# Kernel tuning notes

Measured on AMD Instinct MI355X. Metric: run time of the kernel, lower is better.

The kernel has to match this reference:

```python
import jax, jax.numpy as jnp
import numpy as np

D_MODEL = 1024
N_HEADS = 16
D_K = D_MODEL // N_HEADS
THETA = 10000.0
MAX_SEQ_LEN = 2048


def _rope_tables(seq_len):
    pos = jnp.arange(seq_len, dtype=jnp.float32)
    inv_freq = 1.0 / (THETA ** (jnp.arange(0, D_K, 2, dtype=jnp.float32) / D_K))
    ang = pos[:, None] * inv_freq[None, :]  # [T, D_K/2]
    return jnp.cos(ang), jnp.sin(ang)


def _apply_rope(x, cos, sin):
    # x: [..., T, D_K]; cos/sin: [T, D_K/2]
    x_even = x[..., ::2]
    x_odd = x[..., 1::2]
    r_even = x_even * cos - x_odd * sin
    r_odd = x_even * sin + x_odd * cos
    out = jnp.stack([r_even, r_odd], axis=-1)  # [..., T, D_K/2, 2]
    return out.reshape(x.shape)


def setup_inputs() -> dict:
    key = jax.random.key(0)
    ks = jax.random.split(key, 5)
    std = np.sqrt(2.0 / (D_MODEL + D_MODEL))
    x = jax.random.normal(ks[0], (2, 2048, D_MODEL), dtype=jnp.float32)
    w_q = jax.random.normal(ks[1], (D_MODEL, D_MODEL), dtype=jnp.float32) * std
    w_k = jax.random.normal(ks[2], (D_MODEL, D_MODEL), dtype=jnp.float32) * std
    w_v = jax.random.normal(ks[3], (D_MODEL, D_MODEL), dtype=jnp.float32) * std
    w_o = jax.random.normal(ks[4], (D_MODEL, D_MODEL), dtype=jnp.float32) * std
    return {"x": x, "w_q": w_q, "w_k": w_k, "w_v": w_v, "w_o": w_o}


def reference(x, w_q, w_k, w_v, w_o):
    B, T, _ = x.shape
    # projections: weight stored as [d_out, d_in], y = x @ W^T
    q = jnp.einsum('btd,od->bto', x, w_q)
    k = jnp.einsum('btd,od->bto', x, w_k)
    v = jnp.einsum('btd,od->bto', x, w_v)
    # split heads: [B, T, H*Dk] -> [B, H, T, Dk]
    q = q.reshape(B, T, N_HEADS, D_K).transpose(0, 2, 1, 3)
    k = k.reshape(B, T, N_HEADS, D_K).transpose(0, 2, 1, 3)
    v = v.reshape(B, T, N_HEADS, D_K).transpose(0, 2, 1, 3)
    cos, sin = _rope_tables(T)
    q = _apply_rope(q, cos, sin)
    k = _apply_rope(k, cos, sin)
    scores = jnp.einsum('bhqd,bhkd->bhqk', q, k) / np.sqrt(D_K).astype(np.float32)
    causal = jnp.tril(jnp.ones((T, T), dtype=bool))
    scores = jnp.where(causal, scores, -jnp.inf)
    attn = jax.nn.softmax(scores, axis=-1)
    out = jnp.einsum('bhqk,bhkd->bhqd', attn, v)
    out = out.transpose(0, 2, 1, 3).reshape(B, T, D_MODEL)
    return jnp.einsum('btd,od->bto', out, w_o)
```

## Files before the change

### kernel.cpp

```cpp
#include <hip/hip_runtime.h>
#include <hip/hip_bf16.h>

typedef __bf16 bf16_t;
typedef __bf16 bf16x8 __attribute__((ext_vector_type(8)));
typedef float f32x4 __attribute__((ext_vector_type(4)));
typedef short short4v __attribute__((ext_vector_type(4)));
typedef unsigned int uint2v __attribute__((ext_vector_type(2)));

#define D_MODEL 1024
#define T_SEQ 2048
#define NH 16
#define DKD 64
#define X_ELEMS (4194304u)
#define W_ELEMS (1048576u)
#define Q_SCALE 0.18033688011112042f

__device__ __forceinline__ void async16(const bf16_t* g, bf16_t* l) {
    __builtin_amdgcn_global_load_lds((const __attribute__((address_space(1))) void*)g,
                                     (__attribute__((address_space(3))) void*)l, 16, 0, 0);
}

__device__ __forceinline__ unsigned ldsa(const bf16_t* p) {
    return (unsigned)(size_t)(const __attribute__((address_space(3))) bf16_t*)p;
}

__global__ __launch_bounds__(256) void convert_kernel(
    const float* __restrict__ x, const float* __restrict__ wq,
    const float* __restrict__ wk, const float* __restrict__ wv,
    const float* __restrict__ wo,
    bf16_t* __restrict__ xb, bf16_t* __restrict__ wqb, bf16_t* __restrict__ wkb,
    bf16_t* __restrict__ wvb, bf16_t* __restrict__ wob,
    float* __restrict__ cost, float* __restrict__ sint)
{
    const unsigned bid = blockIdx.x;
    if (bid < 8192) {
        size_t idx = ((size_t)bid * 256 + threadIdx.x) * 4;
        const float* src; bf16_t* dst; size_t off;
        if (idx < X_ELEMS) { src = x; dst = xb; off = idx; }
        else {
            size_t r = idx - X_ELEMS;
            unsigned w = (unsigned)(r >> 20);
            off = r & (W_ELEMS - 1);
            src = (w == 0) ? wq : (w == 1) ? wk : (w == 2) ? wv : wo;
            dst = (w == 0) ? wqb : (w == 1) ? wkb : (w == 2) ? wvb : wob;
        }
        float4 v = *(const float4*)(src + off);
        union { bf16_t b[4]; short4v s; } u;
        u.b[0] = (bf16_t)v.x; u.b[1] = (bf16_t)v.y;
        u.b[2] = (bf16_t)v.z; u.b[3] = (bf16_t)v.w;
        *(short4v*)(dst + off) = u.s;
    } else {
        int idx = (int)(bid - 8192) * 256 + threadIdx.x;
        int t = idx >> 5, i = idx & 31;
        float inv = expf(-0.28782313662425572f * (float)i);
        float ang = (float)t * inv;
        float s, c;
        sincosf(ang, &s, &c);
        cost[idx] = c; sint[idx] = s;
    }
}

__global__ __launch_bounds__(256) void gemm_fused(
    const bf16_t* __restrict__ A,
    const bf16_t* __restrict__ W0, const bf16_t* __restrict__ W1, const bf16_t* __restrict__ W2,
    bf16_t* __restrict__ qout, bf16_t* __restrict__ kout, bf16_t* __restrict__ vout,
    const float* __restrict__ cost, const float* __restrict__ sint,
    float* __restrict__ fout, int modeBase)
{
    const int K = 1024;
    __shared__ bf16_t As[128 * 32];
    __shared__ bf16_t Bs[128 * 32];
    const int tid = threadIdx.x;
    const int wave = tid >> 6, lane = tid & 63;
    const int quad = lane >> 4, l16 = lane & 15;
    const int m0 = blockIdx.x * 128;
    const int n0 = blockIdx.y * 128;
    const int wm = (wave >> 1) * 64, wn = (wave & 1) * 64;
    const int mode = modeBase + blockIdx.z;
    const bf16_t* W = (mode == 1) ? W1 : (mode == 2) ? W2 : W0;

    const bf16_t* Afrag = (mode == 2) ? Bs : As;
    const bf16_t* Bfrag = (mode == 2) ? As : Bs;
    const int aoff = (mode == 2) ? wn : wm;
    const int boff = (mode == 2) ? wm : wn;

    const f32x4 fzero = {0.f, 0.f, 0.f, 0.f};
    f32x4 acc[4][4];
    #pragma unroll
    for (int i = 0; i < 4; ++i)
        #pragma unroll
        for (int j = 0; j < 4; ++j) acc[i][j] = fzero;

    for (int k0 = 0; k0 < K; k0 += 32) {
        __syncthreads();
        #pragma unroll
        for (int c = 0; c < 2; ++c) {
            int G = c * 256 + tid;
            int row = G >> 2, go = G & 3;
            async16(A + (size_t)(m0 + row) * K + (k0 + go * 8), As + (size_t)(c * 256 + wave * 64) * 8);
            async16(W + (size_t)(n0 + row) * K + (k0 + go * 8), Bs + (size_t)(c * 256 + wave * 64) * 8);
        }
        __syncthreads();
        bf16x8 af[4], bfv[4];
        #pragma unroll
        for (int mi = 0; mi < 4; ++mi)
            af[mi] = *(const bf16x8*)(Afrag + (aoff + mi * 16 + l16) * 32 + quad * 8);
        #pragma unroll
        for (int ni = 0; ni < 4; ++ni)
            bfv[ni] = *(const bf16x8*)(Bfrag + (boff + ni * 16 + l16) * 32 + quad * 8);
        #pragma unroll
        for (int mi = 0; mi < 4; ++mi)
            #pragma unroll
            for (int ni = 0; ni < 4; ++ni)
                acc[mi][ni] = __builtin_amdgcn_mfma_f32_16x16x32_bf16(af[mi], bfv[ni], acc[mi][ni], 0, 0, 0);
    }

    #pragma unroll
    for (int mi = 0; mi < 4; ++mi) {
        #pragma unroll
        for (int ni = 0; ni < 4; ++ni) {
            #pragma unroll
            for (int reg = 0; reg < 4; ++reg) {
                float v = acc[mi][ni][reg];
                if (mode == 2) {
                    int f   = n0 + wn + mi * 16 + quad * 4 + reg;
                    int tok = m0 + wm + ni * 16 + l16;
                    int t = tok & (T_SEQ - 1), b = tok >> 11;
                    int h = f >> 6, dk = f & 63;
                    vout[(((size_t)b * NH + h) * DKD + dk) * T_SEQ + t] = (bf16_t)v;
                } else {
                    int row = m0 + wm + mi * 16 + quad * 4 + reg;
                    int col = n0 + wn + ni * 16 + l16;
                    if (mode == 3) {
                        fout[(size_t)row * D_MODEL + col] = v;
                    } else {
                        int t = row & (T_SEQ - 1), b = row >> 11;
                        int h = col >> 6, dk = col & 63;
                        float vp = __shfl_xor(v, 1);
                        int fi = dk >> 1;
                        float c = cost[t * 32 + fi], s = sint[t * 32 + fi];
                        float r = (dk & 1) ? (vp * s + v * c) : (v * c - vp * s);
                        if (mode == 0) r *= Q_SCALE;
                        bf16_t* dst = (mode == 0) ? qout : kout;
                        dst[(((size_t)b * NH + h) * T_SEQ + t) * DKD + dk] = (bf16_t)r;
                    }
                }
            }
        }
    }
}

__global__ __launch_bounds__(256) void out_proj(
    const bf16_t* __restrict__ A, const bf16_t* __restrict__ W,
    float* __restrict__ fout)
{
    const int K = 1024;
    __shared__ bf16_t As[64 * 32];
    __shared__ bf16_t Bs[128 * 32];
    const int tid = threadIdx.x;
    const int wave = tid >> 6, lane = tid & 63;
    const int quad = lane >> 4, l16 = lane & 15;
    const int m0 = blockIdx.x * 64;
    const int n0 = blockIdx.y * 128;
    const int wm = (wave >> 1) * 32, wn = (wave & 1) * 64;

    const f32x4 fzero = {0.f, 0.f, 0.f, 0.f};
    f32x4 acc[2][4];
    #pragma unroll
    for (int i = 0; i < 2; ++i)
        #pragma unroll
        for (int j = 0; j < 4; ++j) acc[i][j] = fzero;

    const int arow = tid >> 2, ago = tid & 3;

    for (int k0 = 0; k0 < K; k0 += 32) {
        __syncthreads();
        async16(A + (size_t)(m0 + arow) * K + (k0 + ago * 8), As + (size_t)(wave * 64) * 8);
        #pragma unroll
        for (int c = 0; c < 2; ++c) {
            int G = c * 256 + tid;
            int row = G >> 2, go = G & 3;
            async16(W + (size_t)(n0 + row) * K + (k0 + go * 8), Bs + (size_t)(c * 256 + wave * 64) * 8);
        }
        __syncthreads();
        bf16x8 af[2], bfv[4];
        #pragma unroll
        for (int mi = 0; mi < 2; ++mi)
            af[mi] = *(const bf16x8*)(As + (wm + mi * 16 + l16) * 32 + quad * 8);
        #pragma unroll
        for (int ni = 0; ni < 4; ++ni)
            bfv[ni] = *(const bf16x8*)(Bs + (wn + ni * 16 + l16) * 32 + quad * 8);
        #pragma unroll
        for (int mi = 0; mi < 2; ++mi)
            #pragma unroll
            for (int ni = 0; ni < 4; ++ni)
                acc[mi][ni] = __builtin_amdgcn_mfma_f32_16x16x32_bf16(af[mi], bfv[ni], acc[mi][ni], 0, 0, 0);
    }

    #pragma unroll
    for (int mi = 0; mi < 2; ++mi) {
        #pragma unroll
        for (int ni = 0; ni < 4; ++ni) {
            #pragma unroll
            for (int reg = 0; reg < 4; ++reg) {
                int row = m0 + wm + mi * 16 + quad * 4 + reg;
                int col = n0 + wn + ni * 16 + l16;
                fout[(size_t)row * D_MODEL + col] = acc[mi][ni][reg];
            }
        }
    }
}

__global__ __launch_bounds__(256, 4) void attn_kernel(
    const bf16_t* __restrict__ Q, const bf16_t* __restrict__ Kb,
    const bf16_t* __restrict__ Vt, bf16_t* __restrict__ O,
    float* __restrict__ Opart, float* __restrict__ Lpart)
{
    __shared__ bf16_t Vs[2][4096];
    __shared__ bf16_t Ks[2][4096];
    const int tid = threadIdx.x;
    const int w = tid >> 6;
    const int lane = tid & 63;
    const int quad = lane >> 4, l16 = lane & 15;
    const int sig = ((quad & 1) << 1) | (quad >> 1);
    const int m7 = l16 & 7;
    const int bh = blockIdx.x;

    int v = 39 - (int)blockIdx.y;
    int g = 0, po = 0;
    for (;; ++g) {
        const int C = (g + 4) >> 2;
        if (v < C) break;
        v -= C;
        if (g >= 4) po += C;
    }
    const int c = v;
    const int ktlo = 8 * c;
    const int kthi = min(8 * c + 8, 2 * g + 2);
    const int qw = (4 * g + w) * 32;

    const bf16_t* kbase = Kb + (size_t)bh * T_SEQ * DKD;
    const bf16_t* vbase = Vt + (size_t)bh * DKD * T_SEQ;

    const int srow = tid >> 3;
    const int sgr  = (tid & 7) ^ (srow & 7);
    const bf16_t* vsrc = vbase + (size_t)srow * T_SEQ + sgr * 8;
    const bf16_t* ksrc = kbase + (size_t)srow * DKD + sgr * 8;

    const unsigned o0  = (unsigned)((l16 * 64 + ((sig ^ m7) * 8)) << 1);
    const unsigned o1  = (unsigned)((l16 * 64 + (((sig + 4) ^ m7) * 8)) << 1);
    const unsigned ko0 = (unsigned)((l16 * 64 + ((quad ^ m7) * 8)) << 1);
    const unsigned ko1 = (unsigned)((l16 * 64 + (((quad + 4) ^ m7) * 8)) << 1);
    const unsigned vb0 = ldsa(Vs[0]), vb1 = ldsa(Vs[1]);
    const unsigned kb0 = ldsa(Ks[0]), kb1 = ldsa(Ks[1]);

    bf16x8 qf[2][2];
    #pragma unroll
    for (int j = 0; j < 2; ++j) {
        const bf16_t* qp = Q + ((size_t)bh * T_SEQ + qw + j * 16 + l16) * DKD;
        qf[j][0] = *(const bf16x8*)(qp + quad * 8);
        qf[j][1] = *(const bf16x8*)(qp + 32 + quad * 8);
    }
    const f32x4 fzero = {0.f, 0.f, 0.f, 0.f};
    f32x4 oacc[2][4];
    #pragma unroll
    for (int j = 0; j < 2; ++j)
        #pragma unroll
        for (int i = 0; i < 4; ++i) oacc[j][i] = fzero;
    float lsum[2] = {0.f, 0.f};

    {
        const bf16_t* vs_ = vsrc + ktlo * 64;
        const bf16_t* ks_ = ksrc + (size_t)ktlo * 64 * DKD;
        async16(vs_,         &Vs[0][0] + w * 512);
        async16(vs_ + 65536, &Vs[0][0] + 2048 + w * 512);
        async16(ks_,         &Ks[0][0] + w * 512);
        async16(ks_ + 2048,  &Ks[0][0] + 2048 + w * 512);
    }
    asm volatile("s_waitcnt vmcnt(0)" ::: "memory");
    __syncthreads();

#define ATT_TILE(VNP, KNP, VCA, KCA) do { \
    const int k0 = kt * 64; \
    if (kt + 1 < kthi) { \
        const bf16_t* vs_ = vsrc + (k0 + 64); \
        const bf16_t* ks_ = ksrc + (size_t)(k0 + 64) * DKD; \
        async16(vs_,         (VNP) + w * 512); \
        async16(vs_ + 65536, (VNP) + 2048 + w * 512); \
        async16(ks_,         (KNP) + w * 512); \
        async16(ks_ + 2048,  (KNP) + 2048 + w * 512); \
    } \
    __builtin_amdgcn_sched_barrier(0); \
    bf16x8 kc00, kc01, kc10, kc11, kc20, kc21, kc30, kc31; \
    { const unsigned kaA = (KCA) + ko0, kaB = (KCA) + ko1; \
      asm volatile( \
        "ds_read_b128 %0, %8 offset:0\n\t" \
        "ds_read_b128 %1, %9 offset:0\n\t" \
        "ds_read_b128 %2, %8 offset:2048\n\t" \
        "ds_read_b128 %3, %9 offset:2048\n\t" \
        "ds_read_b128 %4, %8 offset:4096\n\t" \
        "ds_read_b128 %5, %9 offset:4096\n\t" \
        "ds_read_b128 %6, %8 offset:6144\n\t" \
        "ds_read_b128 %7, %9 offset:6144\n\t" \
        "s_waitcnt lgkmcnt(0)" \
        : "=&v"(kc00), "=&v"(kc01), "=&v"(kc10), "=&v"(kc11), \
          "=&v"(kc20), "=&v"(kc21), "=&v"(kc30), "=&v"(kc31) \
        : "v"(kaA), "v"(kaB)); } \
    __builtin_amdgcn_sched_barrier(0); \
    _Pragma("unroll") \
    for (int j = 0; j < 2; ++j) { \
      if (k0 <= qw + j * 16 + 15) {    \
        const int qcol = qw + j * 16 + l16; \
        f32x4 s[4]; \
        s[0] = __builtin_amdgcn_mfma_f32_16x16x32_bf16(kc00, qf[j][0], fzero, 0, 0, 0); \
        s[0] = __builtin_amdgcn_mfma_f32_16x16x32_bf16(kc01, qf[j][1], s[0], 0, 0, 0); \
        s[1] = __builtin_amdgcn_mfma_f32_16x16x32_bf16(kc10, qf[j][0], fzero, 0, 0, 0); \
        s[1] = __builtin_amdgcn_mfma_f32_16x16x32_bf16(kc11, qf[j][1], s[1], 0, 0, 0); \
        s[2] = __builtin_amdgcn_mfma_f32_16x16x32_bf16(kc20, qf[j][0], fzero, 0, 0, 0); \
        s[2] = __builtin_amdgcn_mfma_f32_16x16x32_bf16(kc21, qf[j][1], s[2], 0, 0, 0); \
        s[3] = __builtin_amdgcn_mfma_f32_16x16x32_bf16(kc30, qf[j][0], fzero, 0, 0, 0); \
        s[3] = __builtin_amdgcn_mfma_f32_16x16x32_bf16(kc31, qf[j][1], s[3], 0, 0, 0); \
        if (k0 + 63 > qw + j * 16) { \
            _Pragma("unroll") \
            for (int fi = 0; fi < 4; ++fi) \
                _Pragma("unroll") \
                for (int reg = 0; reg < 4; ++reg) { \
                    int key = k0 + fi * 16 + quad * 4 + reg; \
                    s[fi][reg] = (key > qcol) ? -__builtin_inff() : s[fi][reg]; \
                } \
        } \
        float sm = 0.f; \
        _Pragma("unroll") \
        for (int fi = 0; fi < 4; ++fi) \
            _Pragma("unroll") \
            for (int reg = 0; reg < 4; ++reg) { \
                float p = __builtin_amdgcn_exp2f(s[fi][reg]); \
                s[fi][reg] = p; sm += p; \
            } \
        lsum[j] += sm; \
        unsigned wv[4][2]; \
        _Pragma("unroll") \
        for (int fi = 0; fi < 4; ++fi) { \
            asm("v_cvt_pk_bf16_f32 %0, %1, %2" : "=v"(wv[fi][0]) : "v"(s[fi][0]), "v"(s[fi][1])); \
            asm("v_cvt_pk_bf16_f32 %0, %1, %2" : "=v"(wv[fi][1]) : "v"(s[fi][2]), "v"(s[fi][3])); \
        } \
        uint2v r0 = __builtin_amdgcn_permlane16_swap(wv[0][0], wv[1][0], false, false); \
        uint2v r1 = __builtin_amdgcn_permlane16_swap(wv[0][1], wv[1][1], false, false); \
        uint2v r2 = __builtin_amdgcn_permlane16_swap(wv[2][0], wv[3][0], false, false); \
        uint2v r3 = __builtin_amdgcn_permlane16_swap(wv[2][1], wv[3][1], false, false); \
        union { unsigned uu[4]; bf16x8 vv; } p0, p1; \
        p0.uu[0] = r0[0]; p0.uu[1] = r1[0]; p0.uu[2] = r0[1]; p0.uu[3] = r1[1]; \
        p1.uu[0] = r2[0]; p1.uu[1] = r3[0]; p1.uu[2] = r2[1]; p1.uu[3] = r3[1]; \
        const unsigned vA = (VCA) + o0, vB = (VCA) + o1; \
        bf16x8 w0a, w0b, w1a, w1b; \
        __builtin_amdgcn_sched_barrier(0); \
        asm volatile( \
            "ds_read_b128 %0, %4 offset:0\n\t" \
            "ds_read_b128 %1, %5 offset:0\n\t" \
            "ds_read_b128 %2, %4 offset:2048\n\t" \
            "ds_read_b128 %3, %5 offset:2048\n\t" \
            "s_waitcnt lgkmcnt(0)" \
            : "=&v"(w0a), "=&v"(w0b), "=&v"(w1a), "=&v"(w1b) \
            : "v"(vA), "v"(vB)); \
        __builtin_amdgcn_sched_barrier(0); \
        oacc[j][0] = __builtin_amdgcn_mfma_f32_16x16x32_bf16(w0a, p0.vv, oacc[j][0], 0, 0, 0); \
        oacc[j][0] = __builtin_amdgcn_mfma_f32_16x16x32_bf16(w0b, p1.vv, oacc[j][0], 0, 0, 0); \
        oacc[j][1] = __builtin_amdgcn_mfma_f32_16x16x32_bf16(w1a, p0.vv, oacc[j][1], 0, 0, 0); \
        oacc[j][1] = __builtin_amdgcn_mfma_f32_16x16x32_bf16(w1b, p1.vv, oacc[j][1], 0, 0, 0); \
        bf16x8 w2a, w2b, w3a, w3b; \
        asm volatile( \
            "ds_read_b128 %0, %4 offset:4096\n\t" \
            "ds_read_b128 %1, %5 offset:4096\n\t" \
            "ds_read_b128 %2, %4 offset:6144\n\t" \
            "ds_read_b128 %3, %5 offset:6144\n\t" \
            "s_waitcnt lgkmcnt(0)" \
            : "=&v"(w2a), "=&v"(w2b), "=&v"(w3a), "=&v"(w3b) \
            : "v"(vA), "v"(vB)); \
        __builtin_amdgcn_sched_barrier(0); \
        oacc[j][2] = __builtin_amdgcn_mfma_f32_16x16x32_bf16(w2a, p0.vv, oacc[j][2], 0, 0, 0); \
        oacc[j][2] = __builtin_amdgcn_mfma_f32_16x16x32_bf16(w2b, p1.vv, oacc[j][2], 0, 0, 0); \
        oacc[j][3] = __builtin_amdgcn_mfma_f32_16x16x32_bf16(w3a, p0.vv, oacc[j][3], 0, 0, 0); \
        oacc[j][3] = __builtin_amdgcn_mfma_f32_16x16x32_bf16(w3b, p1.vv, oacc[j][3], 0, 0, 0); \
      } \
    } \
    asm volatile("s_waitcnt vmcnt(0)" ::: "memory"); \
    __syncthreads(); \
} while (0)

    bool flip = false;
    for (int kt = ktlo; kt < kthi; ++kt) {
        if (!flip) { ATT_TILE(&Vs[1][0], &Ks[1][0], vb0, kb0); }
        else       { ATT_TILE(&Vs[0][0], &Ks[0][0], vb1, kb1); }
        flip = !flip;
    }
#undef ATT_TILE

    if (g < 4) {
        const int b = bh >> 4, h = bh & 15;
        #pragma unroll
        for (int j = 0; j < 2; ++j) {
            float l = lsum[j];
            l += __shfl_xor(l, 16);
            l += __shfl_xor(l, 32);
            float rl = 1.0f / l;
            int q = qw + j * 16 + l16;
            #pragma unroll
            for (int di = 0; di < 4; ++di) {
                union { bf16_t hh[4]; unsigned long long u64; } ok;
                #pragma unroll
                for (int reg = 0; reg < 4; ++reg) ok.hh[reg] = (bf16_t)(oacc[j][di][reg] * rl);
                int d = di * 16 + quad * 4;
                *(unsigned long long*)(O + ((size_t)b * T_SEQ + q) * D_MODEL + h * DKD + d) = ok.u64;
            }
        }
    } else {
        const size_t slot = (size_t)bh * 36 + po + c;
        float* op = Opart + slot * 8192 + (size_t)w * 2048;
        #pragma unroll
        for (int j = 0; j < 2; ++j) {
            Lpart[slot * 512 + w * 128 + j * 64 + lane] = lsum[j];
            #pragma unroll
            for (int di = 0; di < 4; ++di)
                *(f32x4*)(op + ((size_t)(j * 4 + di) * 64 + lane) * 4) = oacc[j][di];
        }
    }
}

__global__ __launch_bounds__(256) void combine_kernel(
    const float* __restrict__ Opart, const float* __restrict__ Lpart, bf16_t* __restrict__ O)
{
    const int bh = blockIdx.x;
    const int g = 4 + blockIdx.y;
    const int C = (g + 4) >> 2;
    int po0 = 0;
    for (int gg = 4; gg < g; ++gg) po0 += (gg + 4) >> 2;
    const int t = threadIdx.x;
    const int ql = t >> 3;
    const int d0 = (t & 7) * 8;
    const int j = ql >> 4, l16 = ql & 15;
    const int di = d0 >> 4;
    const int quad0 = (d0 & 15) >> 2;
    const int b = bh >> 4, h = bh & 15;
    const size_t sb = (size_t)bh * 36 + po0;

    for (int w = 0; w < 4; ++w) {
        float l = 0.f;
        for (int cc = 0; cc < C; ++cc) {
            const float* L = Lpart + (sb + cc) * 512 + w * 128 + j * 64 + l16;
            #pragma unroll
            for (int q = 0; q < 4; ++q) l += L[q * 16];
        }
        const float rl = 1.0f / l;
        union { bf16_t hh[8]; bf16x8 vv; } ov;
        #pragma unroll
        for (int g2 = 0; g2 < 2; ++g2) {
            const int off = ((j * 4 + di) * 64 + (quad0 + g2) * 16 + l16) * 4;
            f32x4 acc = {0.f, 0.f, 0.f, 0.f};
            for (int cc = 0; cc < C; ++cc)
                acc += *(const f32x4*)(Opart + (sb + cc) * 8192 + (size_t)w * 2048 + off);
            #pragma unroll
            for (int reg = 0; reg < 4; ++reg)
                ov.hh[g2 * 4 + reg] = (bf16_t)(acc[reg] * rl);
        }
        const int q = g * 128 + w * 32 + ql;
        *(bf16x8*)(O + ((size_t)b * T_SEQ + q) * D_MODEL + h * DKD + d0) = ov.vv;
    }
}

extern "C" void kernel_launch(void* const* d_in, const int* in_sizes, int n_in,
                              void* d_out, int out_size, void* d_ws, size_t ws_size,
                              hipStream_t stream)
{
    const float* x  = (const float*)d_in[0];
    const float* wq = (const float*)d_in[1];
    const float* wk = (const float*)d_in[2];
    const float* wv = (const float*)d_in[3];
    const float* wo = (const float*)d_in[4];
    float* out = (float*)d_out;

    char* ws = (char*)d_ws;
    size_t off = 0;
    auto alloc = [&](size_t bytes) -> void* {
        void* p = ws + off; off += (bytes + 255) & ~(size_t)255; return p;
    };
    bf16_t* xb   = (bf16_t*)alloc((size_t)X_ELEMS * 2);
    bf16_t* wqb  = (bf16_t*)alloc((size_t)W_ELEMS * 2);
    bf16_t* wkb  = (bf16_t*)alloc((size_t)W_ELEMS * 2);
    bf16_t* wvb  = (bf16_t*)alloc((size_t)W_ELEMS * 2);
    bf16_t* wob  = (bf16_t*)alloc((size_t)W_ELEMS * 2);
    bf16_t* qb   = (bf16_t*)alloc((size_t)X_ELEMS * 2);
    bf16_t* kb   = (bf16_t*)alloc((size_t)X_ELEMS * 2);
    bf16_t* vtb  = (bf16_t*)alloc((size_t)X_ELEMS * 2);
    bf16_t* ob   = (bf16_t*)alloc((size_t)X_ELEMS * 2);
    float*  cost = (float*)alloc((size_t)T_SEQ * 32 * 4);
    float*  sint = (float*)alloc((size_t)T_SEQ * 32 * 4);
    float*  opart = (float*)alloc((size_t)32 * 36 * 8192 * 4);
    float*  lpart = (float*)alloc((size_t)32 * 36 * 512 * 4);

    convert_kernel<<<8448, 256, 0, stream>>>(x, wq, wk, wv, wo, xb, wqb, wkb, wvb, wob,
                                             cost, sint);
    gemm_fused<<<dim3(32, 8, 3), 256, 0, stream>>>(xb, wqb, wkb, wvb, qb, kb, vtb, cost, sint, nullptr, 0);
    attn_kernel<<<dim3(32, 40), 256, 0, stream>>>(qb, kb, vtb, ob, opart, lpart);
    combine_kernel<<<dim3(32, 12), 256, 0, stream>>>(opart, lpart, ob);
    out_proj<<<dim3(64, 8), 256, 0, stream>>>(ob, wob, out);
}
```

Before: 196.5 us.

## Shrink QKV GEMM N-tile to 64 and vectorize transposed V stores

The QKV projection GEMM now uses 128x64 tiles instead of 128x128, doubling the grid to 1536 blocks so more of the GPU's compute units stay busy. The V-output path no longer swaps the A/B fragments; it packs four consecutive tokens per lane into one 64-bit store to the transposed V layout. This aims to improve occupancy and store efficiency, at the cost of more global reloads of the activation tile and lower MFMA reuse per block.

After: 198.9 us. Within noise of the previous version (+1.2%).

```diff
diff --git a/kernel.cpp b/kernel.cpp
--- a/kernel.cpp
+++ b/kernel.cpp
@@ -60,36 +60,30 @@
     }
 }
 
-__global__ __launch_bounds__(256) void gemm_fused(
+__global__ __launch_bounds__(256) void qkv_gemm(
     const bf16_t* __restrict__ A,
     const bf16_t* __restrict__ W0, const bf16_t* __restrict__ W1, const bf16_t* __restrict__ W2,
     bf16_t* __restrict__ qout, bf16_t* __restrict__ kout, bf16_t* __restrict__ vout,
-    const float* __restrict__ cost, const float* __restrict__ sint,
-    float* __restrict__ fout, int modeBase)
+    const float* __restrict__ cost, const float* __restrict__ sint)
 {
     const int K = 1024;
     __shared__ bf16_t As[128 * 32];
-    __shared__ bf16_t Bs[128 * 32];
+    __shared__ bf16_t Bs[64 * 32];
     const int tid = threadIdx.x;
     const int wave = tid >> 6, lane = tid & 63;
     const int quad = lane >> 4, l16 = lane & 15;
     const int m0 = blockIdx.x * 128;
-    const int n0 = blockIdx.y * 128;
-    const int wm = (wave >> 1) * 64, wn = (wave & 1) * 64;
-    const int mode = modeBase + blockIdx.z;
+    const int n0 = blockIdx.y * 64;
+    const int wm = (wave >> 1) * 64, wn = (wave & 1) * 32;
+    const int mode = blockIdx.z;
     const bf16_t* W = (mode == 1) ? W1 : (mode == 2) ? W2 : W0;
 
-    const bf16_t* Afrag = (mode == 2) ? Bs : As;
-    const bf16_t* Bfrag = (mode == 2) ? As : Bs;
-    const int aoff = (mode == 2) ? wn : wm;
-    const int boff = (mode == 2) ? wm : wn;
-
     const f32x4 fzero = {0.f, 0.f, 0.f, 0.f};
-    f32x4 acc[4][4];
+    f32x4 acc[4][2];
     #pragma unroll
     for (int i = 0; i < 4; ++i)
         #pragma unroll
-        for (int j = 0; j < 4; ++j) acc[i][j] = fzero;
+        for (int j = 0; j < 2; ++j) acc[i][j] = fzero;
 
     for (int k0 = 0; k0 < K; k0 += 32) {
         __syncthreads();
@@ -98,52 +92,54 @@
             int G = c * 256 + tid;
             int row = G >> 2, go = G & 3;
             async16(A + (size_t)(m0 + row) * K + (k0 + go * 8), As + (size_t)(c * 256 + wave * 64) * 8);
-            async16(W + (size_t)(n0 + row) * K + (k0 + go * 8), Bs + (size_t)(c * 256 + wave * 64) * 8);
+        }
+        {
+            int row = tid >> 2, go = tid & 3;
+            async16(W + (size_t)(n0 + row) * K + (k0 + go * 8), Bs + (size_t)(wave * 64) * 8);
         }
         __syncthreads();
-        bf16x8 af[4], bfv[4];
+        bf16x8 af[4], bfv[2];
         #pragma unroll
         for (int mi = 0; mi < 4; ++mi)
-            af[mi] = *(const bf16x8*)(Afrag + (aoff + mi * 16 + l16) * 32 + quad * 8);
-        #pragma unroll
-        for (int ni = 0; ni < 4; ++ni)
-            bfv[ni] = *(const bf16x8*)(Bfrag + (boff + ni * 16 + l16) * 32 + quad * 8);
+            af[mi] = *(const bf16x8*)(As + (wm + mi * 16 + l16) * 32 + quad * 8);
+        #pragma unroll
+        for (int ni = 0; ni < 2; ++ni)
+            bfv[ni] = *(const bf16x8*)(Bs + (wn + ni * 16 + l16) * 32 + quad * 8);
         #pragma unroll
         for (int mi = 0; mi < 4; ++mi)
             #pragma unroll
-            for (int ni = 0; ni < 4; ++ni)
+            for (int ni = 0; ni < 2; ++ni)
                 acc[mi][ni] = __builtin_amdgcn_mfma_f32_16x16x32_bf16(af[mi], bfv[ni], acc[mi][ni], 0, 0, 0);
     }
 
     #pragma unroll
     for (int mi = 0; mi < 4; ++mi) {
         #pragma unroll
-        for (int ni = 0; ni < 4; ++ni) {
-            #pragma unroll
-            for (int reg = 0; reg < 4; ++reg) {
-                float v = acc[mi][ni][reg];
-                if (mode == 2) {
-                    int f   = n0 + wn + mi * 16 + quad * 4 + reg;
-                    int tok = m0 + wm + ni * 16 + l16;
-                    int t = tok & (T_SEQ - 1), b = tok >> 11;
-                    int h = f >> 6, dk = f & 63;
-                    vout[(((size_t)b * NH + h) * DKD + dk) * T_SEQ + t] = (bf16_t)v;
-                } else {
+        for (int ni = 0; ni < 2; ++ni) {
+            if (mode == 2) {
+                int col = n0 + wn + ni * 16 + l16;
+                int row0 = m0 + wm + mi * 16 + quad * 4;
+                int t0 = row0 & (T_SEQ - 1), b = row0 >> 11;
+                int h = col >> 6, dk = col & 63;
+                union { bf16_t hh[4]; unsigned long long u64; } pk;
+                #pragma unroll
+                for (int reg = 0; reg < 4; ++reg) pk.hh[reg] = (bf16_t)acc[mi][ni][reg];
+                *(unsigned long long*)(vout + (((size_t)b * NH + h) * DKD + dk) * T_SEQ + t0) = pk.u64;
+            } else {
+                #pragma unroll
+                for (int reg = 0; reg < 4; ++reg) {
+                    float v = acc[mi][ni][reg];
                     int row = m0 + wm + mi * 16 + quad * 4 + reg;
                     int col = n0 + wn + ni * 16 + l16;
-                    if (mode == 3) {
-                        fout[(size_t)row * D_MODEL + col] = v;
-                    } else {
-                        int t = row & (T_SEQ - 1), b = row >> 11;
-                        int h = col >> 6, dk = col & 63;
-                        float vp = __shfl_xor(v, 1);
-                        int fi = dk >> 1;
-                        float c = cost[t * 32 + fi], s = sint[t * 32 + fi];
-                        float r = (dk & 1) ? (vp * s + v * c) : (v * c - vp * s);
-                        if (mode == 0) r *= Q_SCALE;
-                        bf16_t* dst = (mode == 0) ? qout : kout;
-                        dst[(((size_t)b * NH + h) * T_SEQ + t) * DKD + dk] = (bf16_t)r;
-                    }
+                    int t = row & (T_SEQ - 1), b = row >> 11;
+                    int h = col >> 6, dk = col & 63;
+                    float vp = __shfl_xor(v, 1);
+                    int fi = dk >> 1;
+                    float c = cost[t * 32 + fi], s = sint[t * 32 + fi];
+                    float r = (dk & 1) ? (vp * s + v * c) : (v * c - vp * s);
+                    if (mode == 0) r *= Q_SCALE;
+                    bf16_t* dst = (mode == 0) ? qout : kout;
+                    dst[(((size_t)b * NH + h) * T_SEQ + t) * DKD + dk] = (bf16_t)r;
                 }
             }
         }
@@ -499,7 +495,7 @@
 
     convert_kernel<<<8448, 256, 0, stream>>>(x, wq, wk, wv, wo, xb, wqb, wkb, wvb, wob,
                                              cost, sint);
-    gemm_fused<<<dim3(32, 8, 3), 256, 0, stream>>>(xb, wqb, wkb, wvb, qb, kb, vtb, cost, sint, nullptr, 0);
+    qkv_gemm<<<dim3(32, 16, 3), 256, 0, stream>>>(xb, wqb, wkb, wvb, qb, kb, vtb, cost, sint);
     attn_kernel<<<dim3(32, 40), 256, 0, stream>>>(qb, kb, vtb, ob, opart, lpart);
     combine_kernel<<<dim3(32, 12), 256, 0, stream>>>(opart, lpart, ob);
     out_proj<<<dim3(64, 8), 256, 0, stream>>>(ob, wob, out);
```
